# Kernel tuning notes

Measured on AMD Instinct MI355X. Metric: run time of the kernel, lower is better.

Reference implementation:

```python
import jax, jax.numpy as jnp
import numpy as np

N_STEPS = 20  # ceil((t1-t0)/dt0) with dt0=0.05 on [0,1]


def setup_inputs() -> dict:
    key = jax.random.key(0)
    ks = jax.random.split(key, 12)
    B, D, H, VF, LS, LAB = 512, 5, 128, 256, 63, 10
    Lm1 = LS - 1  # 62, effective logsig dim after dropping channel 0
    ts = jnp.linspace(0.0, 1.0, 33, dtype=jnp.float32)
    intervals = jnp.linspace(0.0, 1.0, 33, dtype=jnp.float32)
    logsig = jax.random.normal(ks[0], (32, LS), dtype=jnp.float32)
    x0 = jax.random.normal(ks[1], (B, D), dtype=jnp.float32)
    def lin(k, fan_in, shape):
        return jax.random.uniform(k, shape, jnp.float32, -1.0, 1.0) / np.sqrt(fan_in)
    return {
        "ts": ts, "logsig": logsig, "x0": x0, "intervals": intervals,
        "W_vf1": lin(ks[2], H, (VF, H)),  "b_vf1": lin(ks[3], H, (VF,)),
        "W_vf2": lin(ks[4], VF, (VF, VF)), "b_vf2": lin(ks[5], VF, (VF,)),
        "W_m": lin(ks[6], VF, (H * Lm1, VF)), "b_m": lin(ks[7], VF, (H * Lm1,)),
        "W_in": lin(ks[8], D, (H, D)),   "b_in": lin(ks[9], D, (H,)),
        "W_out": lin(ks[10], H, (LAB, H)), "b_out": lin(ks[11], H, (LAB,)),
    }


def reference(ts, logsig, x0, intervals, W_vf1, b_vf1, W_vf2, b_vf2,
              W_m, b_m, W_in, b_in, W_out, b_out):
    B = x0.shape[0]
    H = W_in.shape[0]
    L = logsig.shape[1] - 1  # channel 0 dropped

    def vector_field(t, y):
        # locate interval containing t (torch.searchsorted default = left)
        idx = jnp.clip(jnp.searchsorted(intervals[1:], t) + 1, 1, intervals.shape[0] - 1)
        seg = logsig[idx - 1, 1:]                     # (L,)
        h = jax.nn.relu(y @ W_vf1.T + b_vf1)          # (B, VF)
        h = jnp.tanh(h @ W_vf2.T + b_vf2)             # (B, VF) final_activation=tanh
        m = (h @ W_m.T + b_m).reshape(B, H, L)        # (B, H, L)
        dydt = jnp.einsum('bhl,l->bh', m, seg)
        return dydt / (intervals[idx] - intervals[idx - 1])

    y0 = x0 @ W_in.T + b_in                           # linear1
    t0, t1 = ts[0], ts[-1]
    dt = (t1 - t0) / N_STEPS

    def heun_step(y, i):
        t = t0 + i * dt
        k1 = vector_field(t, y)
        k2 = vector_field(t + dt, y + dt * k1)
        return y + 0.5 * dt * (k1 + k2), None

    yT, _ = jax.lax.scan(heun_step, y0, jnp.arange(N_STEPS, dtype=jnp.float32))
    return jax.nn.softmax(yT @ W_out.T + b_out, axis=-1)
```

## Files before the change

### kernel.cpp

```cpp
#include <hip/hip_runtime.h>

#define AW 264
#define YW 136

typedef _Float16 f16x8 __attribute__((ext_vector_type(8)));
typedef _Float16 f16x4 __attribute__((ext_vector_type(4)));
typedef __attribute__((ext_vector_type(4))) float f32x4;

__device__ __forceinline__ float fast_tanh(float x) {
    float e = __expf(2.0f * x);
    return 1.0f - 2.0f / (e + 1.0f);
}
__device__ __forceinline__ void bar_lds() {
    asm volatile("s_waitcnt lgkmcnt(0)\n\ts_barrier" ::: "memory");
}

__global__ __launch_bounds__(256) void pk_all(
    const float* __restrict__ Wvf1, const float* __restrict__ Wvf2,
    const float* __restrict__ Wm,   const float* __restrict__ bm,
    const float* __restrict__ logsig,
    _Float16* __restrict__ W1F, _Float16* __restrict__ W2F,
    _Float16* __restrict__ A3F, float* __restrict__ c_all)
{
    __shared__ float ls[32][62];
    const int b = blockIdx.x, t = threadIdx.x;
    if (b < 128) {
        int u = b * 256 + t;
        int j = u & 7, l = (u >> 3) & 63;
        int kc = (u >> 9) & 3, nt = (u >> 9) >> 2;
        int n = nt * 16 + (l & 15), k = kc * 32 + (l >> 4) * 8 + j;
        float w = Wvf1[n * 128 + k];
        _Float16 hi = (_Float16)w;
        W1F[u] = hi;
        W1F[32768 + u] = (_Float16)(w - (float)hi);
    } else if (b < 384) {
        int u = (b - 128) * 256 + t;
        int j = u & 7, l = (u >> 3) & 63;
        int kc = (u >> 9) & 7, nt = (u >> 9) >> 3;
        int n = nt * 16 + (l & 15), k = kc * 32 + (l >> 4) * 8 + j;
        float w = Wvf2[n * 256 + k];
        _Float16 hi = (_Float16)w;
        W2F[u] = hi;
        W2F[65536 + u] = (_Float16)(w - (float)hi);
    } else if (b < 896) {
        for (int e2 = t; e2 < 32 * 62; e2 += 256)
            ls[e2 / 62][e2 % 62] = logsig[(e2 / 62) * 63 + 1 + (e2 % 62)];
        __syncthreads();
        int idx = b - 384;
        int chunk = idx >> 7;
        int u = (idx & 127) * 256 + t;
        int j = u & 7, l = (u >> 3) & 63, kc = (u >> 9) & 7, nt = (u >> 12) & 7;
        int h = nt * 16 + (l & 15);
        int v = kc * 32 + (l >> 4) * 8 + j;
        int r0 = chunk * 8;
        float acc[8];
#pragma unroll
        for (int r = 0; r < 8; r++) acc[r] = 0.f;
        for (int ll = 0; ll < 62; ll++) {
            float wv2 = Wm[(h * 62 + ll) * 256 + v];
#pragma unroll
            for (int r = 0; r < 8; r++) acc[r] += wv2 * ls[r0 + r][ll];
        }
        for (int r = 0; r < 8; r++) {
            _Float16 hi = (_Float16)acc[r];
            A3F[(r0 + r) * 65536 + u] = hi;
            A3F[(r0 + r) * 65536 + 32768 + u] = (_Float16)(acc[r] - (float)hi);
        }
    } else {
        int u = (b - 896) * 256 + t;
        int r = u >> 7, h = u & 127;
        float acc = 0.f;
        for (int ll = 0; ll < 62; ll++) acc += bm[h * 62 + ll] * logsig[r * 63 + 1 + ll];
        c_all[u] = acc;
    }
}

__global__ __launch_bounds__(512, 2) void rde_main(
    const float* __restrict__ ts, const float* __restrict__ x0,
    const float* __restrict__ intervals,
    const float* __restrict__ b1g, const float* __restrict__ b2g,
    const float* __restrict__ Win, const float* __restrict__ bin,
    const float* __restrict__ Wout, const float* __restrict__ bout,
    const _Float16* __restrict__ W1F, const _Float16* __restrict__ W2F,
    const _Float16* __restrict__ A3F, const float* __restrict__ c_all,
    float* __restrict__ out)
{
    __shared__ __align__(16) _Float16 W1s[65536];
    __shared__ __align__(16) _Float16 AH[16 * AW], AL[16 * AW];
    __shared__ float Ys[16 * YW];
    __shared__ float ivl[33];
    __shared__ int   r_arr[40];
    __shared__ float s_arr[40];
    __shared__ float lg[16][12];

    const int t    = threadIdx.x;
    const int lane = t & 63;
    const int wv   = t >> 6;
    const int m16  = lane & 15;
    const int q    = lane >> 4;
    const int row0 = blockIdx.x * 16;

    if (t < 33) ivl[t] = intervals[t];
    for (int e2 = t; e2 < 8192; e2 += 512)
        ((uint4*)W1s)[e2] = ((const uint4*)W1F)[e2];
    __syncthreads();

    const float ts0 = ts[0];
    const float dt  = __fdiv_rn(ts[32] - ts0, 20.0f);

    if (t < 40) {
        int i = t >> 1;
        float tv = ts0 + (float)i * dt;
        if (t & 1) tv += dt;
        int p = 0;
        for (int j2 = 0; j2 < 32; j2++) p += (ivl[1 + j2] < tv) ? 1 : 0;
        int idx = p + 1;
        idx = idx < 1 ? 1 : idx;
        idx = idx > 32 ? 32 : idx;
        r_arr[t] = idx - 1;
        s_arr[t] = __fdiv_rn(1.0f, ivl[idx] - ivl[idx - 1]);
    }

    f32x4 b1f[2], b2f[2];
#pragma unroll
    for (int tt = 0; tt < 2; tt++) {
        b1f[tt] = *(const f32x4*)(b1g + (wv * 2 + tt) * 16 + q * 4);
        b2f[tt] = *(const f32x4*)(b2g + (wv * 2 + tt) * 16 + q * 4);
    }

    float Y[4], K1[4];
    {
        const float* xr = x0 + (row0 + m16) * 5;
        float xv[5];
#pragma unroll
        for (int d = 0; d < 5; d++) xv[d] = xr[d];
        int h0 = wv * 16 + q * 4;
        f16x4 hv, lv;
#pragma unroll
        for (int r = 0; r < 4; r++) {
            float acc = bin[h0 + r];
#pragma unroll
            for (int d = 0; d < 5; d++) acc += xv[d] * Win[(h0 + r) * 5 + d];
            Y[r] = acc;
            K1[r] = 0.f;
            _Float16 hi = (_Float16)acc;
            hv[r] = hi;
            lv[r] = (_Float16)(acc - (float)hi);
        }
        *(f16x4*)(AH + m16 * AW + h0) = hv;
        *(f16x4*)(AL + m16 * AW + h0) = lv;
    }
    __syncthreads();

#pragma unroll 1
    for (int e = 0; e < 40; e++) {
        const int half = e & 1;
        const int ri   = r_arr[e];
        const float s  = s_arr[e];
        const _Float16* ABase = A3F + ri * 65536;

        f16x8 w2a[2][4][2];
#pragma unroll
        for (int tt = 0; tt < 2; tt++)
#pragma unroll
            for (int kc = 0; kc < 4; kc++) {
                const _Float16* bp = W2F + (((wv * 2 + tt) * 8 + kc) * 64 + lane) * 8;
                w2a[tt][kc][0] = *(const f16x8*)bp;
                w2a[tt][kc][1] = *(const f16x8*)(bp + 65536);
            }
        f32x4 aA[2], aB[2], aC[2];
#pragma unroll
        for (int tt = 0; tt < 2; tt++) {
            aA[tt] = b1f[tt];
            aB[tt] = (f32x4){0.f, 0.f, 0.f, 0.f};
            aC[tt] = (f32x4){0.f, 0.f, 0.f, 0.f};
        }
#pragma unroll
        for (int kc = 0; kc < 4; kc++) {
            int ao = m16 * AW + kc * 32 + q * 8;
            f16x8 ah = *(const f16x8*)(AH + ao);
            f16x8 al = *(const f16x8*)(AL + ao);
#pragma unroll
            for (int tt = 0; tt < 2; tt++) {
                int wb = (((wv * 2 + tt) * 4 + kc) * 64 + lane) * 8;
                f16x8 bh = *(const f16x8*)(W1s + wb);
                f16x8 bl = *(const f16x8*)(W1s + 32768 + wb);
                aA[tt] = __builtin_amdgcn_mfma_f32_16x16x32_f16(bh, ah, aA[tt], 0, 0, 0);
                aB[tt] = __builtin_amdgcn_mfma_f32_16x16x32_f16(bl, ah, aB[tt], 0, 0, 0);
                aC[tt] = __builtin_amdgcn_mfma_f32_16x16x32_f16(bh, al, aC[tt], 0, 0, 0);
            }
        }
        bar_lds();
#pragma unroll
        for (int tt = 0; tt < 2; tt++) {
            int n0 = (wv * 2 + tt) * 16 + q * 4;
            f16x4 hv, lv;
#pragma unroll
            for (int r = 0; r < 4; r++) {
                float v = fmaxf(aA[tt][r] + aB[tt][r] + aC[tt][r], 0.f);
                _Float16 hi = (_Float16)v;
                hv[r] = hi;
                lv[r] = (_Float16)(v - (float)hi);
            }
            *(f16x4*)(AH + m16 * AW + n0) = hv;
            *(f16x4*)(AL + m16 * AW + n0) = lv;
        }
        bar_lds();

        f16x8 w2b[2][4][2];
#pragma unroll
        for (int tt = 0; tt < 2; tt++)
#pragma unroll
            for (int kc = 0; kc < 4; kc++) {
                const _Float16* bp = W2F + (((wv * 2 + tt) * 8 + 4 + kc) * 64 + lane) * 8;
                w2b[tt][kc][0] = *(const f16x8*)bp;
                w2b[tt][kc][1] = *(const f16x8*)(bp + 65536);
            }
#pragma unroll
        for (int tt = 0; tt < 2; tt++) {
            aA[tt] = b2f[tt];
            aB[tt] = (f32x4){0.f, 0.f, 0.f, 0.f};
            aC[tt] = (f32x4){0.f, 0.f, 0.f, 0.f};
        }
#pragma unroll
        for (int kc = 0; kc < 4; kc++) {
            int ao = m16 * AW + kc * 32 + q * 8;
            f16x8 ah = *(const f16x8*)(AH + ao);
            f16x8 al = *(const f16x8*)(AL + ao);
#pragma unroll
            for (int tt = 0; tt < 2; tt++) {
                aA[tt] = __builtin_amdgcn_mfma_f32_16x16x32_f16(w2a[tt][kc][0], ah, aA[tt], 0, 0, 0);
                aB[tt] = __builtin_amdgcn_mfma_f32_16x16x32_f16(w2a[tt][kc][1], ah, aB[tt], 0, 0, 0);
                aC[tt] = __builtin_amdgcn_mfma_f32_16x16x32_f16(w2a[tt][kc][0], al, aC[tt], 0, 0, 0);
            }
        }
        f16x8 a3a[4][2];
#pragma unroll
        for (int kc = 0; kc < 4; kc++) {
            const _Float16* bp = ABase + ((wv * 8 + kc) * 64 + lane) * 8;
            a3a[kc][0] = *(const f16x8*)bp;
            a3a[kc][1] = *(const f16x8*)(bp + 32768);
        }
        f32x4 cf = *(const f32x4*)(c_all + ri * 128 + wv * 16 + q * 4);
#pragma unroll
        for (int kc = 0; kc < 4; kc++) {
            int ao = m16 * AW + (4 + kc) * 32 + q * 8;
            f16x8 ah = *(const f16x8*)(AH + ao);
            f16x8 al = *(const f16x8*)(AL + ao);
#pragma unroll
            for (int tt = 0; tt < 2; tt++) {
                aA[tt] = __builtin_amdgcn_mfma_f32_16x16x32_f16(w2b[tt][kc][0], ah, aA[tt], 0, 0, 0);
                aB[tt] = __builtin_amdgcn_mfma_f32_16x16x32_f16(w2b[tt][kc][1], ah, aB[tt], 0, 0, 0);
                aC[tt] = __builtin_amdgcn_mfma_f32_16x16x32_f16(w2b[tt][kc][0], al, aC[tt], 0, 0, 0);
            }
        }
        f16x8 a3b[4][2];
#pragma unroll
        for (int kc = 0; kc < 4; kc++) {
            const _Float16* bp = ABase + ((wv * 8 + 4 + kc) * 64 + lane) * 8;
            a3b[kc][0] = *(const f16x8*)bp;
            a3b[kc][1] = *(const f16x8*)(bp + 32768);
        }
        bar_lds();
#pragma unroll
        for (int tt = 0; tt < 2; tt++) {
            int n0 = (wv * 2 + tt) * 16 + q * 4;
            f16x4 hv, lv;
#pragma unroll
            for (int r = 0; r < 4; r++) {
                float v = fast_tanh(aA[tt][r] + aB[tt][r] + aC[tt][r]);
                _Float16 hi = (_Float16)v;
                hv[r] = hi;
                lv[r] = (_Float16)(v - (float)hi);
            }
            *(f16x4*)(AH + m16 * AW + n0) = hv;
            *(f16x4*)(AL + m16 * AW + n0) = lv;
        }
        bar_lds();

        f32x4 kA = cf;
        f32x4 kB = (f32x4){0.f, 0.f, 0.f, 0.f};
        f32x4 kC = (f32x4){0.f, 0.f, 0.f, 0.f};
#pragma unroll
        for (int kc = 0; kc < 4; kc++) {
            int ao = m16 * AW + kc * 32 + q * 8;
            f16x8 ah = *(const f16x8*)(AH + ao);
            f16x8 al = *(const f16x8*)(AL + ao);
            kA = __builtin_amdgcn_mfma_f32_16x16x32_f16(a3a[kc][0], ah, kA, 0, 0, 0);
            kB = __builtin_amdgcn_mfma_f32_16x16x32_f16(a3a[kc][1], ah, kB, 0, 0, 0);
            kC = __builtin_amdgcn_mfma_f32_16x16x32_f16(a3a[kc][0], al, kC, 0, 0, 0);
        }
#pragma unroll
        for (int kc = 0; kc < 4; kc++) {
            int ao = m16 * AW + (4 + kc) * 32 + q * 8;
            f16x8 ah = *(const f16x8*)(AH + ao);
            f16x8 al = *(const f16x8*)(AL + ao);
            kA = __builtin_amdgcn_mfma_f32_16x16x32_f16(a3b[kc][0], ah, kA, 0, 0, 0);
            kB = __builtin_amdgcn_mfma_f32_16x16x32_f16(a3b[kc][1], ah, kB, 0, 0, 0);
            kC = __builtin_amdgcn_mfma_f32_16x16x32_f16(a3b[kc][0], al, kC, 0, 0, 0);
        }
        bar_lds();
        {
            int h0 = wv * 16 + q * 4;
            f16x4 hv, lv;
#pragma unroll
            for (int r = 0; r < 4; r++) {
                float kv = (kA[r] + kB[r] + kC[r]) * s;
                float yn;
                if (half == 0) {
                    K1[r] = kv;
                    yn = Y[r] + dt * kv;
                } else {
                    yn = Y[r] + 0.5f * dt * (K1[r] + kv);
                    Y[r] = yn;
                }
                _Float16 hi = (_Float16)yn;
                hv[r] = hi;
                lv[r] = (_Float16)(yn - (float)hi);
            }
            *(f16x4*)(AH + m16 * AW + h0) = hv;
            *(f16x4*)(AL + m16 * AW + h0) = lv;
        }
        bar_lds();
    }

#pragma unroll
    for (int r = 0; r < 4; r++)
        Ys[m16 * YW + wv * 16 + q * 4 + r] = Y[r];
    __syncthreads();
    if (t < 160) {
        int m = t / 10, c = t % 10;
        float acc = bout[c];
        for (int k = 0; k < 128; k++) acc += Ys[m * YW + k] * Wout[c * 128 + k];
        lg[m][c] = acc;
    }
    __syncthreads();
    if (t < 16) {
        float mx = -1e30f;
#pragma unroll
        for (int c = 0; c < 10; c++) mx = fmaxf(mx, lg[t][c]);
        float ex[10], sum = 0.f;
#pragma unroll
        for (int c = 0; c < 10; c++) { ex[c] = expf(lg[t][c] - mx); sum += ex[c]; }
        float inv = __fdiv_rn(1.0f, sum);
#pragma unroll
        for (int c = 0; c < 10; c++) out[(row0 + t) * 10 + c] = ex[c] * inv;
    }
}

extern "C" void kernel_launch(void* const* d_in, const int* in_sizes, int n_in,
                              void* d_out, int out_size, void* d_ws, size_t ws_size,
                              hipStream_t stream) {
    const float* ts     = (const float*)d_in[0];
    const float* logsig = (const float*)d_in[1];
    const float* x0     = (const float*)d_in[2];
    const float* ivls   = (const float*)d_in[3];
    const float* Wvf1   = (const float*)d_in[4];
    const float* bvf1   = (const float*)d_in[5];
    const float* Wvf2   = (const float*)d_in[6];
    const float* bvf2   = (const float*)d_in[7];
    const float* Wm     = (const float*)d_in[8];
    const float* bm     = (const float*)d_in[9];
    const float* Win    = (const float*)d_in[10];
    const float* bin    = (const float*)d_in[11];
    const float* Wout   = (const float*)d_in[12];
    const float* bout   = (const float*)d_in[13];

    _Float16* W1F = (_Float16*)d_ws;
    _Float16* W2F = W1F + 65536;
    _Float16* A3F = W2F + 131072;
    float* c_all = (float*)(A3F + 32 * 65536);
    float* out = (float*)d_out;

    pk_all<<<dim3(912), dim3(256), 0, stream>>>(Wvf1, Wvf2, Wm, bm, logsig,
                                                W1F, W2F, A3F, c_all);
    rde_main<<<dim3(32), dim3(512), 0, stream>>>(
        ts, x0, ivls, bvf1, bvf2, Win, bin, Wout, bout,
        W1F, W2F, A3F, c_all, out);
}
```

Baseline: 269.1 us.

## Ping-pong LDS activation buffers, keep W1 in registers, restructure A3 precompute

The main loop now alternates between two LDS activation buffer pairs, which lets it drop two of the four barriers per vector-field evaluation. The W1 split-fp16 fragments are now loaded once into registers instead of being staged in LDS, which removes the per-iteration LDS reads for the first layer. The pack kernel computes all 32 logsig rows per thread, cutting the block count and the redundant re-reads of Wm. The costs are much higher register pressure in rde_main under launch_bounds(512,2), with possible spills, and fewer parallel blocks in the precompute.

```diff
diff --git a/kernel.cpp b/kernel.cpp
--- a/kernel.cpp
+++ b/kernel.cpp
@@ -6,6 +6,7 @@
 typedef _Float16 f16x8 __attribute__((ext_vector_type(8)));
 typedef _Float16 f16x4 __attribute__((ext_vector_type(4)));
 typedef __attribute__((ext_vector_type(4))) float f32x4;
+typedef __attribute__((ext_vector_type(2))) float f32x2;
 
 __device__ __forceinline__ float fast_tanh(float x) {
     float e = __expf(2.0f * x);
@@ -42,32 +43,35 @@
         _Float16 hi = (_Float16)w;
         W2F[u] = hi;
         W2F[65536 + u] = (_Float16)(w - (float)hi);
-    } else if (b < 896) {
+    } else if (b < 512) {
         for (int e2 = t; e2 < 32 * 62; e2 += 256)
             ls[e2 / 62][e2 % 62] = logsig[(e2 / 62) * 63 + 1 + (e2 % 62)];
         __syncthreads();
-        int idx = b - 384;
-        int chunk = idx >> 7;
-        int u = (idx & 127) * 256 + t;
+        int u = (b - 384) * 256 + t;
         int j = u & 7, l = (u >> 3) & 63, kc = (u >> 9) & 7, nt = (u >> 12) & 7;
         int h = nt * 16 + (l & 15);
         int v = kc * 32 + (l >> 4) * 8 + j;
-        int r0 = chunk * 8;
-        float acc[8];
-#pragma unroll
-        for (int r = 0; r < 8; r++) acc[r] = 0.f;
-        for (int ll = 0; ll < 62; ll++) {
-            float wv2 = Wm[(h * 62 + ll) * 256 + v];
-#pragma unroll
-            for (int r = 0; r < 8; r++) acc[r] += wv2 * ls[r0 + r][ll];
-        }
-        for (int r = 0; r < 8; r++) {
+        float acc[32];
+#pragma unroll
+        for (int r = 0; r < 32; r++) acc[r] = 0.f;
+        const float* wp = Wm + (h * 62) * 256 + v;
+        for (int ll = 0; ll < 62; ll += 2) {
+            float w0 = wp[ll * 256];
+            float w1 = wp[ll * 256 + 256];
+#pragma unroll
+            for (int r = 0; r < 32; r++) {
+                f32x2 lv = *(const f32x2*)&ls[r][ll];
+                acc[r] += w0 * lv.x + w1 * lv.y;
+            }
+        }
+#pragma unroll
+        for (int r = 0; r < 32; r++) {
             _Float16 hi = (_Float16)acc[r];
-            A3F[(r0 + r) * 65536 + u] = hi;
-            A3F[(r0 + r) * 65536 + 32768 + u] = (_Float16)(acc[r] - (float)hi);
+            A3F[r * 65536 + u] = hi;
+            A3F[r * 65536 + 32768 + u] = (_Float16)(acc[r] - (float)hi);
         }
     } else {
-        int u = (b - 896) * 256 + t;
+        int u = (b - 512) * 256 + t;
         int r = u >> 7, h = u & 127;
         float acc = 0.f;
         for (int ll = 0; ll < 62; ll++) acc += bm[h * 62 + ll] * logsig[r * 63 + 1 + ll];
@@ -85,8 +89,7 @@
     const _Float16* __restrict__ A3F, const float* __restrict__ c_all,
     float* __restrict__ out)
 {
-    __shared__ __align__(16) _Float16 W1s[65536];
-    __shared__ __align__(16) _Float16 AH[16 * AW], AL[16 * AW];
+    __shared__ __align__(16) _Float16 ABUF[4][16 * AW];
     __shared__ float Ys[16 * YW];
     __shared__ float ivl[33];
     __shared__ int   r_arr[40];
@@ -100,9 +103,17 @@
     const int q    = lane >> 4;
     const int row0 = blockIdx.x * 16;
 
+    f16x8 w1h[2][4], w1l[2][4];
+#pragma unroll
+    for (int tt = 0; tt < 2; tt++)
+#pragma unroll
+        for (int kc = 0; kc < 4; kc++) {
+            const _Float16* p = W1F + (((wv * 2 + tt) * 4 + kc) * 64 + lane) * 8;
+            w1h[tt][kc] = *(const f16x8*)p;
+            w1l[tt][kc] = *(const f16x8*)(p + 32768);
+        }
+
     if (t < 33) ivl[t] = intervals[t];
-    for (int e2 = t; e2 < 8192; e2 += 512)
-        ((uint4*)W1s)[e2] = ((const uint4*)W1F)[e2];
     __syncthreads();
 
     const float ts0 = ts[0];
@@ -147,14 +158,12 @@
             hv[r] = hi;
             lv[r] = (_Float16)(acc - (float)hi);
         }
-        *(f16x4*)(AH + m16 * AW + h0) = hv;
-        *(f16x4*)(AL + m16 * AW + h0) = lv;
+        *(f16x4*)(&ABUF[0][m16 * AW + h0]) = hv;
+        *(f16x4*)(&ABUF[1][m16 * AW + h0]) = lv;
     }
     __syncthreads();
 
-#pragma unroll 1
-    for (int e = 0; e < 40; e++) {
-        const int half = e & 1;
+    auto EVAL = [&](int e, int half, int pb, int qb) {
         const int ri   = r_arr[e];
         const float s  = s_arr[e];
         const _Float16* ABase = A3F + ri * 65536;
@@ -178,19 +187,15 @@
 #pragma unroll
         for (int kc = 0; kc < 4; kc++) {
             int ao = m16 * AW + kc * 32 + q * 8;
-            f16x8 ah = *(const f16x8*)(AH + ao);
-            f16x8 al = *(const f16x8*)(AL + ao);
+            f16x8 ah = *(const f16x8*)(&ABUF[pb][ao]);
+            f16x8 al = *(const f16x8*)(&ABUF[pb + 1][ao]);
 #pragma unroll
             for (int tt = 0; tt < 2; tt++) {
-                int wb = (((wv * 2 + tt) * 4 + kc) * 64 + lane) * 8;
-                f16x8 bh = *(const f16x8*)(W1s + wb);
-                f16x8 bl = *(const f16x8*)(W1s + 32768 + wb);
-                aA[tt] = __builtin_amdgcn_mfma_f32_16x16x32_f16(bh, ah, aA[tt], 0, 0, 0);
-                aB[tt] = __builtin_amdgcn_mfma_f32_16x16x32_f16(bl, ah, aB[tt], 0, 0, 0);
-                aC[tt] = __builtin_amdgcn_mfma_f32_16x16x32_f16(bh, al, aC[tt], 0, 0, 0);
-            }
-        }
-        bar_lds();
+                aA[tt] = __builtin_amdgcn_mfma_f32_16x16x32_f16(w1h[tt][kc], ah, aA[tt], 0, 0, 0);
+                aB[tt] = __builtin_amdgcn_mfma_f32_16x16x32_f16(w1l[tt][kc], ah, aB[tt], 0, 0, 0);
+                aC[tt] = __builtin_amdgcn_mfma_f32_16x16x32_f16(w1h[tt][kc], al, aC[tt], 0, 0, 0);
+            }
+        }
 #pragma unroll
         for (int tt = 0; tt < 2; tt++) {
             int n0 = (wv * 2 + tt) * 16 + q * 4;
@@ -202,8 +207,8 @@
                 hv[r] = hi;
                 lv[r] = (_Float16)(v - (float)hi);
             }
-            *(f16x4*)(AH + m16 * AW + n0) = hv;
-            *(f16x4*)(AL + m16 * AW + n0) = lv;
+            *(f16x4*)(&ABUF[qb][m16 * AW + n0]) = hv;
+            *(f16x4*)(&ABUF[qb + 1][m16 * AW + n0]) = lv;
         }
         bar_lds();
 
@@ -225,8 +230,8 @@
 #pragma unroll
         for (int kc = 0; kc < 4; kc++) {
             int ao = m16 * AW + kc * 32 + q * 8;
-            f16x8 ah = *(const f16x8*)(AH + ao);
-            f16x8 al = *(const f16x8*)(AL + ao);
+            f16x8 ah = *(const f16x8*)(&ABUF[qb][ao]);
+            f16x8 al = *(const f16x8*)(&ABUF[qb + 1][ao]);
 #pragma unroll
             for (int tt = 0; tt < 2; tt++) {
                 aA[tt] = __builtin_amdgcn_mfma_f32_16x16x32_f16(w2a[tt][kc][0], ah, aA[tt], 0, 0, 0);
@@ -245,8 +250,8 @@
 #pragma unroll
         for (int kc = 0; kc < 4; kc++) {
             int ao = m16 * AW + (4 + kc) * 32 + q * 8;
-            f16x8 ah = *(const f16x8*)(AH + ao);
-            f16x8 al = *(const f16x8*)(AL + ao);
+            f16x8 ah = *(const f16x8*)(&ABUF[qb][ao]);
+            f16x8 al = *(const f16x8*)(&ABUF[qb + 1][ao]);
 #pragma unroll
             for (int tt = 0; tt < 2; tt++) {
                 aA[tt] = __builtin_amdgcn_mfma_f32_16x16x32_f16(w2b[tt][kc][0], ah, aA[tt], 0, 0, 0);
@@ -261,7 +266,6 @@
             a3b[kc][0] = *(const f16x8*)bp;
             a3b[kc][1] = *(const f16x8*)(bp + 32768);
         }
-        bar_lds();
 #pragma unroll
         for (int tt = 0; tt < 2; tt++) {
             int n0 = (wv * 2 + tt) * 16 + q * 4;
@@ -273,8 +277,8 @@
                 hv[r] = hi;
                 lv[r] = (_Float16)(v - (float)hi);
             }
-            *(f16x4*)(AH + m16 * AW + n0) = hv;
-            *(f16x4*)(AL + m16 * AW + n0) = lv;
+            *(f16x4*)(&ABUF[pb][m16 * AW + n0]) = hv;
+            *(f16x4*)(&ABUF[pb + 1][m16 * AW + n0]) = lv;
         }
         bar_lds();
 
@@ -284,8 +288,8 @@
 #pragma unroll
         for (int kc = 0; kc < 4; kc++) {
             int ao = m16 * AW + kc * 32 + q * 8;
-            f16x8 ah = *(const f16x8*)(AH + ao);
-            f16x8 al = *(const f16x8*)(AL + ao);
+            f16x8 ah = *(const f16x8*)(&ABUF[pb][ao]);
+            f16x8 al = *(const f16x8*)(&ABUF[pb + 1][ao]);
             kA = __builtin_amdgcn_mfma_f32_16x16x32_f16(a3a[kc][0], ah, kA, 0, 0, 0);
             kB = __builtin_amdgcn_mfma_f32_16x16x32_f16(a3a[kc][1], ah, kB, 0, 0, 0);
             kC = __builtin_amdgcn_mfma_f32_16x16x32_f16(a3a[kc][0], al, kC, 0, 0, 0);
@@ -293,13 +297,12 @@
 #pragma unroll
         for (int kc = 0; kc < 4; kc++) {
             int ao = m16 * AW + (4 + kc) * 32 + q * 8;
-            f16x8 ah = *(const f16x8*)(AH + ao);
-            f16x8 al = *(const f16x8*)(AL + ao);
+            f16x8 ah = *(const f16x8*)(&ABUF[pb][ao]);
+            f16x8 al = *(const f16x8*)(&ABUF[pb + 1][ao]);
             kA = __builtin_amdgcn_mfma_f32_16x16x32_f16(a3b[kc][0], ah, kA, 0, 0, 0);
             kB = __builtin_amdgcn_mfma_f32_16x16x32_f16(a3b[kc][1], ah, kB, 0, 0, 0);
             kC = __builtin_amdgcn_mfma_f32_16x16x32_f16(a3b[kc][0], al, kC, 0, 0, 0);
         }
-        bar_lds();
         {
             int h0 = wv * 16 + q * 4;
             f16x4 hv, lv;
@@ -318,10 +321,16 @@
                 hv[r] = hi;
                 lv[r] = (_Float16)(yn - (float)hi);
             }
-            *(f16x4*)(AH + m16 * AW + h0) = hv;
-            *(f16x4*)(AL + m16 * AW + h0) = lv;
+            *(f16x4*)(&ABUF[qb][m16 * AW + h0]) = hv;
+            *(f16x4*)(&ABUF[qb + 1][m16 * AW + h0]) = lv;
         }
         bar_lds();
+    };
+
+#pragma unroll 1
+    for (int e2 = 0; e2 < 20; e2++) {
+        EVAL(2 * e2,     0, 0, 2);
+        EVAL(2 * e2 + 1, 1, 2, 0);
     }
 
 #pragma unroll
@@ -372,7 +381,7 @@
     float* c_all = (float*)(A3F + 32 * 65536);
     float* out = (float*)d_out;
 
-    pk_all<<<dim3(912), dim3(256), 0, stream>>>(Wvf1, Wvf2, Wm, bm, logsig,
+    pk_all<<<dim3(528), dim3(256), 0, stream>>>(Wvf1, Wvf2, Wm, bm, logsig,
                                                 W1F, W2F, A3F, c_all);
     rde_main<<<dim3(32), dim3(512), 0, stream>>>(
         ts, x0, ivls, bvf1, bvf2, Win, bin, Wout, bout,
```

New measurement: 378.2 us. 40.6% more time.

## Ping-pong activation buffers with fragment layout, cut barriers, keep W1 hi in registers

Applied to the files above, without the earlier changes.

Replaces the single padded AH/AL activation tile with two ping-pong hi/lo buffer pairs stored in MFMA-fragment order, so each stage writes into the other buffer. This lets three of the five LDS barriers per evaluation be removed, because reads and writes no longer alias. The high half of W1 is held in registers and only the low half stays in LDS, which shrinks shared memory. Launch bounds drop to one block per CU, trading occupancy for more registers. The loop is unrolled by two to alternate buffers.

```diff
diff --git a/kernel.cpp b/kernel.cpp
--- a/kernel.cpp
+++ b/kernel.cpp
@@ -1,6 +1,5 @@
 #include <hip/hip_runtime.h>
 
-#define AW 264
 #define YW 136
 
 typedef _Float16 f16x8 __attribute__((ext_vector_type(8)));
@@ -13,6 +12,10 @@
 }
 __device__ __forceinline__ void bar_lds() {
     asm volatile("s_waitcnt lgkmcnt(0)\n\ts_barrier" ::: "memory");
+}
+
+__device__ __forceinline__ int fidx(int m, int c) {
+    return ((c >> 5) << 9) | (((c >> 3) & 3) << 7) | (m << 3) | (c & 7);
 }
 
 __global__ __launch_bounds__(256) void pk_all(
@@ -75,7 +78,7 @@
     }
 }
 
-__global__ __launch_bounds__(512, 2) void rde_main(
+__global__ __launch_bounds__(512, 1) void rde_main(
     const float* __restrict__ ts, const float* __restrict__ x0,
     const float* __restrict__ intervals,
     const float* __restrict__ b1g, const float* __restrict__ b2g,
@@ -85,8 +88,8 @@
     const _Float16* __restrict__ A3F, const float* __restrict__ c_all,
     float* __restrict__ out)
 {
-    __shared__ __align__(16) _Float16 W1s[65536];
-    __shared__ __align__(16) _Float16 AH[16 * AW], AL[16 * AW];
+    __shared__ __align__(16) _Float16 W1L[32768];
+    __shared__ __align__(16) _Float16 ABUF[4][4096];
     __shared__ float Ys[16 * YW];
     __shared__ float ivl[33];
     __shared__ int   r_arr[40];
@@ -100,9 +103,16 @@
     const int q    = lane >> 4;
     const int row0 = blockIdx.x * 16;
 
+    f16x8 w1h[2][4];
+#pragma unroll
+    for (int tt = 0; tt < 2; tt++)
+#pragma unroll
+        for (int kc = 0; kc < 4; kc++)
+            w1h[tt][kc] = *(const f16x8*)(W1F + ((wv * 8 + tt * 4 + kc) * 64 + lane) * 8);
+    for (int e2 = t; e2 < 4096; e2 += 512)
+        ((uint4*)W1L)[e2] = ((const uint4*)(W1F + 32768))[e2];
+
     if (t < 33) ivl[t] = intervals[t];
-    for (int e2 = t; e2 < 8192; e2 += 512)
-        ((uint4*)W1s)[e2] = ((const uint4*)W1F)[e2];
     __syncthreads();
 
     const float ts0 = ts[0];
@@ -134,37 +144,39 @@
         float xv[5];
 #pragma unroll
         for (int d = 0; d < 5; d++) xv[d] = xr[d];
-        int h0 = wv * 16 + q * 4;
+        int c0 = wv * 16 + q * 4;
         f16x4 hv, lv;
 #pragma unroll
         for (int r = 0; r < 4; r++) {
-            float acc = bin[h0 + r];
-#pragma unroll
-            for (int d = 0; d < 5; d++) acc += xv[d] * Win[(h0 + r) * 5 + d];
+            float acc = bin[c0 + r];
+#pragma unroll
+            for (int d = 0; d < 5; d++) acc += xv[d] * Win[(c0 + r) * 5 + d];
             Y[r] = acc;
             K1[r] = 0.f;
             _Float16 hi = (_Float16)acc;
             hv[r] = hi;
             lv[r] = (_Float16)(acc - (float)hi);
         }
-        *(f16x4*)(AH + m16 * AW + h0) = hv;
-        *(f16x4*)(AL + m16 * AW + h0) = lv;
+        *(f16x4*)(ABUF[0] + fidx(m16, c0)) = hv;
+        *(f16x4*)(ABUF[1] + fidx(m16, c0)) = lv;
     }
     __syncthreads();
 
-#pragma unroll 1
-    for (int e = 0; e < 40; e++) {
-        const int half = e & 1;
+    auto EVAL = [&](int e, int half, int pb, int qb) {
         const int ri   = r_arr[e];
         const float s  = s_arr[e];
         const _Float16* ABase = A3F + ri * 65536;
+        _Float16* Ph = ABUF[pb];
+        _Float16* Pl = ABUF[pb + 1];
+        _Float16* Qh = ABUF[qb];
+        _Float16* Ql = ABUF[qb + 1];
 
         f16x8 w2a[2][4][2];
 #pragma unroll
         for (int tt = 0; tt < 2; tt++)
 #pragma unroll
             for (int kc = 0; kc < 4; kc++) {
-                const _Float16* bp = W2F + (((wv * 2 + tt) * 8 + kc) * 64 + lane) * 8;
+                const _Float16* bp = W2F + ((wv * 16 + tt * 8 + kc) * 64 + lane) * 8;
                 w2a[tt][kc][0] = *(const f16x8*)bp;
                 w2a[tt][kc][1] = *(const f16x8*)(bp + 65536);
             }
@@ -177,20 +189,16 @@
         }
 #pragma unroll
         for (int kc = 0; kc < 4; kc++) {
-            int ao = m16 * AW + kc * 32 + q * 8;
-            f16x8 ah = *(const f16x8*)(AH + ao);
-            f16x8 al = *(const f16x8*)(AL + ao);
+            f16x8 ah = *(const f16x8*)(Ph + kc * 512 + lane * 8);
+            f16x8 al = *(const f16x8*)(Pl + kc * 512 + lane * 8);
 #pragma unroll
             for (int tt = 0; tt < 2; tt++) {
-                int wb = (((wv * 2 + tt) * 4 + kc) * 64 + lane) * 8;
-                f16x8 bh = *(const f16x8*)(W1s + wb);
-                f16x8 bl = *(const f16x8*)(W1s + 32768 + wb);
-                aA[tt] = __builtin_amdgcn_mfma_f32_16x16x32_f16(bh, ah, aA[tt], 0, 0, 0);
+                f16x8 bl = *(const f16x8*)(W1L + (wv * 8 + tt * 4 + kc) * 512 + lane * 8);
+                aA[tt] = __builtin_amdgcn_mfma_f32_16x16x32_f16(w1h[tt][kc], ah, aA[tt], 0, 0, 0);
                 aB[tt] = __builtin_amdgcn_mfma_f32_16x16x32_f16(bl, ah, aB[tt], 0, 0, 0);
-                aC[tt] = __builtin_amdgcn_mfma_f32_16x16x32_f16(bh, al, aC[tt], 0, 0, 0);
-            }
-        }
-        bar_lds();
+                aC[tt] = __builtin_amdgcn_mfma_f32_16x16x32_f16(w1h[tt][kc], al, aC[tt], 0, 0, 0);
+            }
+        }
 #pragma unroll
         for (int tt = 0; tt < 2; tt++) {
             int n0 = (wv * 2 + tt) * 16 + q * 4;
@@ -202,8 +210,8 @@
                 hv[r] = hi;
                 lv[r] = (_Float16)(v - (float)hi);
             }
-            *(f16x4*)(AH + m16 * AW + n0) = hv;
-            *(f16x4*)(AL + m16 * AW + n0) = lv;
+            *(f16x4*)(Qh + fidx(m16, n0)) = hv;
+            *(f16x4*)(Ql + fidx(m16, n0)) = lv;
         }
         bar_lds();
 
@@ -212,7 +220,7 @@
         for (int tt = 0; tt < 2; tt++)
 #pragma unroll
             for (int kc = 0; kc < 4; kc++) {
-                const _Float16* bp = W2F + (((wv * 2 + tt) * 8 + 4 + kc) * 64 + lane) * 8;
+                const _Float16* bp = W2F + ((wv * 16 + tt * 8 + 4 + kc) * 64 + lane) * 8;
                 w2b[tt][kc][0] = *(const f16x8*)bp;
                 w2b[tt][kc][1] = *(const f16x8*)(bp + 65536);
             }
@@ -224,9 +232,8 @@
         }
 #pragma unroll
         for (int kc = 0; kc < 4; kc++) {
-            int ao = m16 * AW + kc * 32 + q * 8;
-            f16x8 ah = *(const f16x8*)(AH + ao);
-            f16x8 al = *(const f16x8*)(AL + ao);
+            f16x8 ah = *(const f16x8*)(Qh + kc * 512 + lane * 8);
+            f16x8 al = *(const f16x8*)(Ql + kc * 512 + lane * 8);
 #pragma unroll
             for (int tt = 0; tt < 2; tt++) {
                 aA[tt] = __builtin_amdgcn_mfma_f32_16x16x32_f16(w2a[tt][kc][0], ah, aA[tt], 0, 0, 0);
@@ -244,9 +251,8 @@
         f32x4 cf = *(const f32x4*)(c_all + ri * 128 + wv * 16 + q * 4);
 #pragma unroll
         for (int kc = 0; kc < 4; kc++) {
-            int ao = m16 * AW + (4 + kc) * 32 + q * 8;
-            f16x8 ah = *(const f16x8*)(AH + ao);
-            f16x8 al = *(const f16x8*)(AL + ao);
+            f16x8 ah = *(const f16x8*)(Qh + (4 + kc) * 512 + lane * 8);
+            f16x8 al = *(const f16x8*)(Ql + (4 + kc) * 512 + lane * 8);
 #pragma unroll
             for (int tt = 0; tt < 2; tt++) {
                 aA[tt] = __builtin_amdgcn_mfma_f32_16x16x32_f16(w2b[tt][kc][0], ah, aA[tt], 0, 0, 0);
@@ -261,7 +267,6 @@
             a3b[kc][0] = *(const f16x8*)bp;
             a3b[kc][1] = *(const f16x8*)(bp + 32768);
         }
-        bar_lds();
 #pragma unroll
         for (int tt = 0; tt < 2; tt++) {
             int n0 = (wv * 2 + tt) * 16 + q * 4;
@@ -273,8 +278,8 @@
                 hv[r] = hi;
                 lv[r] = (_Float16)(v - (float)hi);
             }
-            *(f16x4*)(AH + m16 * AW + n0) = hv;
-            *(f16x4*)(AL + m16 * AW + n0) = lv;
+            *(f16x4*)(Ph + fidx(m16, n0)) = hv;
+            *(f16x4*)(Pl + fidx(m16, n0)) = lv;
         }
         bar_lds();
 
@@ -283,25 +288,22 @@
         f32x4 kC = (f32x4){0.f, 0.f, 0.f, 0.f};
 #pragma unroll
         for (int kc = 0; kc < 4; kc++) {
-            int ao = m16 * AW + kc * 32 + q * 8;
-            f16x8 ah = *(const f16x8*)(AH + ao);
-            f16x8 al = *(const f16x8*)(AL + ao);
+            f16x8 ah = *(const f16x8*)(Ph + kc * 512 + lane * 8);
+            f16x8 al = *(const f16x8*)(Pl + kc * 512 + lane * 8);
             kA = __builtin_amdgcn_mfma_f32_16x16x32_f16(a3a[kc][0], ah, kA, 0, 0, 0);
             kB = __builtin_amdgcn_mfma_f32_16x16x32_f16(a3a[kc][1], ah, kB, 0, 0, 0);
             kC = __builtin_amdgcn_mfma_f32_16x16x32_f16(a3a[kc][0], al, kC, 0, 0, 0);
         }
 #pragma unroll
         for (int kc = 0; kc < 4; kc++) {
-            int ao = m16 * AW + (4 + kc) * 32 + q * 8;
-            f16x8 ah = *(const f16x8*)(AH + ao);
-            f16x8 al = *(const f16x8*)(AL + ao);
+            f16x8 ah = *(const f16x8*)(Ph + (4 + kc) * 512 + lane * 8);
+            f16x8 al = *(const f16x8*)(Pl + (4 + kc) * 512 + lane * 8);
             kA = __builtin_amdgcn_mfma_f32_16x16x32_f16(a3b[kc][0], ah, kA, 0, 0, 0);
             kB = __builtin_amdgcn_mfma_f32_16x16x32_f16(a3b[kc][1], ah, kB, 0, 0, 0);
             kC = __builtin_amdgcn_mfma_f32_16x16x32_f16(a3b[kc][0], al, kC, 0, 0, 0);
         }
-        bar_lds();
         {
-            int h0 = wv * 16 + q * 4;
+            int c0 = wv * 16 + q * 4;
             f16x4 hv, lv;
 #pragma unroll
             for (int r = 0; r < 4; r++) {
@@ -318,10 +320,16 @@
                 hv[r] = hi;
                 lv[r] = (_Float16)(yn - (float)hi);
             }
-            *(f16x4*)(AH + m16 * AW + h0) = hv;
-            *(f16x4*)(AL + m16 * AW + h0) = lv;
+            *(f16x4*)(Qh + fidx(m16, c0)) = hv;
+            *(f16x4*)(Ql + fidx(m16, c0)) = lv;
         }
         bar_lds();
+    };
+
+#pragma unroll 1
+    for (int e2 = 0; e2 < 20; e2++) {
+        EVAL(2 * e2,     0, 0, 2);
+        EVAL(2 * e2 + 1, 1, 2, 0);
     }
 
 #pragma unroll
```

New measurement: 316.3 us. 1.18x slower.

## Split activation LDS into separate Y and H buffers in fragment layout, drop barriers

Applied to the files above, without the earlier changes.

Replaces the padded row-major activation buffers with an MFMA-fragment-ordered layout (fidx), so each lane reads its operand with a contiguous lane*8 access. Y and hidden activations now sit in separate buffers, which removes two of the per-stage barriers that guarded write-after-read on the shared buffer. Also unrolls the precompute loops in the packing kernel. Dropping the barriers relies on the Y/H separation being enough to prevent races, and the final epilogue reuses the H buffer as scratch.

```diff
diff --git a/kernel.cpp b/kernel.cpp
--- a/kernel.cpp
+++ b/kernel.cpp
@@ -1,6 +1,5 @@
 #include <hip/hip_runtime.h>
 
-#define AW 264
 #define YW 136
 
 typedef _Float16 f16x8 __attribute__((ext_vector_type(8)));
@@ -13,6 +12,10 @@
 }
 __device__ __forceinline__ void bar_lds() {
     asm volatile("s_waitcnt lgkmcnt(0)\n\ts_barrier" ::: "memory");
+}
+
+__device__ __forceinline__ int fidx(int m, int c) {
+    return ((c >> 5) << 9) | (((c >> 3) & 3) << 7) | (m << 3) | (c & 7);
 }
 
 __global__ __launch_bounds__(256) void pk_all(
@@ -56,11 +59,13 @@
         float acc[8];
 #pragma unroll
         for (int r = 0; r < 8; r++) acc[r] = 0.f;
+#pragma unroll
         for (int ll = 0; ll < 62; ll++) {
             float wv2 = Wm[(h * 62 + ll) * 256 + v];
 #pragma unroll
             for (int r = 0; r < 8; r++) acc[r] += wv2 * ls[r0 + r][ll];
         }
+#pragma unroll
         for (int r = 0; r < 8; r++) {
             _Float16 hi = (_Float16)acc[r];
             A3F[(r0 + r) * 65536 + u] = hi;
@@ -70,6 +75,7 @@
         int u = (b - 896) * 256 + t;
         int r = u >> 7, h = u & 127;
         float acc = 0.f;
+#pragma unroll
         for (int ll = 0; ll < 62; ll++) acc += bm[h * 62 + ll] * logsig[r * 63 + 1 + ll];
         c_all[u] = acc;
     }
@@ -86,12 +92,16 @@
     float* __restrict__ out)
 {
     __shared__ __align__(16) _Float16 W1s[65536];
-    __shared__ __align__(16) _Float16 AH[16 * AW], AL[16 * AW];
-    __shared__ float Ys[16 * YW];
+    __shared__ __align__(16) _Float16 HBUF[2][4096];
+    __shared__ __align__(16) _Float16 YBUF[2][2048];
     __shared__ float ivl[33];
     __shared__ int   r_arr[40];
     __shared__ float s_arr[40];
-    __shared__ float lg[16][12];
+
+    _Float16* Hh = HBUF[0];
+    _Float16* Hl = HBUF[1];
+    _Float16* Yh = YBUF[0];
+    _Float16* Yl = YBUF[1];
 
     const int t    = threadIdx.x;
     const int lane = t & 63;
@@ -134,21 +144,21 @@
         float xv[5];
 #pragma unroll
         for (int d = 0; d < 5; d++) xv[d] = xr[d];
-        int h0 = wv * 16 + q * 4;
+        int c0 = wv * 16 + q * 4;
         f16x4 hv, lv;
 #pragma unroll
         for (int r = 0; r < 4; r++) {
-            float acc = bin[h0 + r];
-#pragma unroll
-            for (int d = 0; d < 5; d++) acc += xv[d] * Win[(h0 + r) * 5 + d];
+            float acc = bin[c0 + r];
+#pragma unroll
+            for (int d = 0; d < 5; d++) acc += xv[d] * Win[(c0 + r) * 5 + d];
             Y[r] = acc;
             K1[r] = 0.f;
             _Float16 hi = (_Float16)acc;
             hv[r] = hi;
             lv[r] = (_Float16)(acc - (float)hi);
         }
-        *(f16x4*)(AH + m16 * AW + h0) = hv;
-        *(f16x4*)(AL + m16 * AW + h0) = lv;
+        *(f16x4*)(Yh + fidx(m16, c0)) = hv;
+        *(f16x4*)(Yl + fidx(m16, c0)) = lv;
     }
     __syncthreads();
 
@@ -164,7 +174,7 @@
         for (int tt = 0; tt < 2; tt++)
 #pragma unroll
             for (int kc = 0; kc < 4; kc++) {
-                const _Float16* bp = W2F + (((wv * 2 + tt) * 8 + kc) * 64 + lane) * 8;
+                const _Float16* bp = W2F + ((wv * 16 + tt * 8 + kc) * 64 + lane) * 8;
                 w2a[tt][kc][0] = *(const f16x8*)bp;
                 w2a[tt][kc][1] = *(const f16x8*)(bp + 65536);
             }
@@ -177,12 +187,11 @@
         }
 #pragma unroll
         for (int kc = 0; kc < 4; kc++) {
-            int ao = m16 * AW + kc * 32 + q * 8;
-            f16x8 ah = *(const f16x8*)(AH + ao);
-            f16x8 al = *(const f16x8*)(AL + ao);
+            f16x8 ah = *(const f16x8*)(Yh + kc * 512 + lane * 8);
+            f16x8 al = *(const f16x8*)(Yl + kc * 512 + lane * 8);
 #pragma unroll
             for (int tt = 0; tt < 2; tt++) {
-                int wb = (((wv * 2 + tt) * 4 + kc) * 64 + lane) * 8;
+                int wb = ((wv * 8 + tt * 4 + kc) * 64 + lane) * 8;
                 f16x8 bh = *(const f16x8*)(W1s + wb);
                 f16x8 bl = *(const f16x8*)(W1s + 32768 + wb);
                 aA[tt] = __builtin_amdgcn_mfma_f32_16x16x32_f16(bh, ah, aA[tt], 0, 0, 0);
@@ -190,7 +199,6 @@
                 aC[tt] = __builtin_amdgcn_mfma_f32_16x16x32_f16(bh, al, aC[tt], 0, 0, 0);
             }
         }
-        bar_lds();
 #pragma unroll
         for (int tt = 0; tt < 2; tt++) {
             int n0 = (wv * 2 + tt) * 16 + q * 4;
@@ -202,8 +210,8 @@
                 hv[r] = hi;
                 lv[r] = (_Float16)(v - (float)hi);
             }
-            *(f16x4*)(AH + m16 * AW + n0) = hv;
-            *(f16x4*)(AL + m16 * AW + n0) = lv;
+            *(f16x4*)(Hh + fidx(m16, n0)) = hv;
+            *(f16x4*)(Hl + fidx(m16, n0)) = lv;
         }
         bar_lds();
 
@@ -212,7 +220,7 @@
         for (int tt = 0; tt < 2; tt++)
 #pragma unroll
             for (int kc = 0; kc < 4; kc++) {
-                const _Float16* bp = W2F + (((wv * 2 + tt) * 8 + 4 + kc) * 64 + lane) * 8;
+                const _Float16* bp = W2F + ((wv * 16 + tt * 8 + 4 + kc) * 64 + lane) * 8;
                 w2b[tt][kc][0] = *(const f16x8*)bp;
                 w2b[tt][kc][1] = *(const f16x8*)(bp + 65536);
             }
@@ -224,9 +232,8 @@
         }
 #pragma unroll
         for (int kc = 0; kc < 4; kc++) {
-            int ao = m16 * AW + kc * 32 + q * 8;
-            f16x8 ah = *(const f16x8*)(AH + ao);
-            f16x8 al = *(const f16x8*)(AL + ao);
+            f16x8 ah = *(const f16x8*)(Hh + kc * 512 + lane * 8);
+            f16x8 al = *(const f16x8*)(Hl + kc * 512 + lane * 8);
 #pragma unroll
             for (int tt = 0; tt < 2; tt++) {
                 aA[tt] = __builtin_amdgcn_mfma_f32_16x16x32_f16(w2a[tt][kc][0], ah, aA[tt], 0, 0, 0);
@@ -244,9 +251,8 @@
         f32x4 cf = *(const f32x4*)(c_all + ri * 128 + wv * 16 + q * 4);
 #pragma unroll
         for (int kc = 0; kc < 4; kc++) {
-            int ao = m16 * AW + (4 + kc) * 32 + q * 8;
-            f16x8 ah = *(const f16x8*)(AH + ao);
-            f16x8 al = *(const f16x8*)(AL + ao);
+            f16x8 ah = *(const f16x8*)(Hh + (4 + kc) * 512 + lane * 8);
+            f16x8 al = *(const f16x8*)(Hl + (4 + kc) * 512 + lane * 8);
 #pragma unroll
             for (int tt = 0; tt < 2; tt++) {
                 aA[tt] = __builtin_amdgcn_mfma_f32_16x16x32_f16(w2b[tt][kc][0], ah, aA[tt], 0, 0, 0);
@@ -273,8 +279,8 @@
                 hv[r] = hi;
                 lv[r] = (_Float16)(v - (float)hi);
             }
-            *(f16x4*)(AH + m16 * AW + n0) = hv;
-            *(f16x4*)(AL + m16 * AW + n0) = lv;
+            *(f16x4*)(Hh + fidx(m16, n0)) = hv;
+            *(f16x4*)(Hl + fidx(m16, n0)) = lv;
         }
         bar_lds();
 
@@ -283,25 +289,22 @@
         f32x4 kC = (f32x4){0.f, 0.f, 0.f, 0.f};
 #pragma unroll
         for (int kc = 0; kc < 4; kc++) {
-            int ao = m16 * AW + kc * 32 + q * 8;
-            f16x8 ah = *(const f16x8*)(AH + ao);
-            f16x8 al = *(const f16x8*)(AL + ao);
+            f16x8 ah = *(const f16x8*)(Hh + kc * 512 + lane * 8);
+            f16x8 al = *(const f16x8*)(Hl + kc * 512 + lane * 8);
             kA = __builtin_amdgcn_mfma_f32_16x16x32_f16(a3a[kc][0], ah, kA, 0, 0, 0);
             kB = __builtin_amdgcn_mfma_f32_16x16x32_f16(a3a[kc][1], ah, kB, 0, 0, 0);
             kC = __builtin_amdgcn_mfma_f32_16x16x32_f16(a3a[kc][0], al, kC, 0, 0, 0);
         }
 #pragma unroll
         for (int kc = 0; kc < 4; kc++) {
-            int ao = m16 * AW + (4 + kc) * 32 + q * 8;
-            f16x8 ah = *(const f16x8*)(AH + ao);
-            f16x8 al = *(const f16x8*)(AL + ao);
+            f16x8 ah = *(const f16x8*)(Hh + (4 + kc) * 512 + lane * 8);
+            f16x8 al = *(const f16x8*)(Hl + (4 + kc) * 512 + lane * 8);
             kA = __builtin_amdgcn_mfma_f32_16x16x32_f16(a3b[kc][0], ah, kA, 0, 0, 0);
             kB = __builtin_amdgcn_mfma_f32_16x16x32_f16(a3b[kc][1], ah, kB, 0, 0, 0);
             kC = __builtin_amdgcn_mfma_f32_16x16x32_f16(a3b[kc][0], al, kC, 0, 0, 0);
         }
-        bar_lds();
         {
-            int h0 = wv * 16 + q * 4;
+            int c0 = wv * 16 + q * 4;
             f16x4 hv, lv;
 #pragma unroll
             for (int r = 0; r < 4; r++) {
@@ -318,12 +321,14 @@
                 hv[r] = hi;
                 lv[r] = (_Float16)(yn - (float)hi);
             }
-            *(f16x4*)(AH + m16 * AW + h0) = hv;
-            *(f16x4*)(AL + m16 * AW + h0) = lv;
+            *(f16x4*)(Yh + fidx(m16, c0)) = hv;
+            *(f16x4*)(Yl + fidx(m16, c0)) = lv;
         }
         bar_lds();
     }
 
+    float* Ys  = (float*)&HBUF[0][0];
+    float* lgp = (float*)&HBUF[0][0] + 16 * YW;
 #pragma unroll
     for (int r = 0; r < 4; r++)
         Ys[m16 * YW + wv * 16 + q * 4 + r] = Y[r];
@@ -332,16 +337,16 @@
         int m = t / 10, c = t % 10;
         float acc = bout[c];
         for (int k = 0; k < 128; k++) acc += Ys[m * YW + k] * Wout[c * 128 + k];
-        lg[m][c] = acc;
+        lgp[m * 10 + c] = acc;
     }
     __syncthreads();
     if (t < 16) {
         float mx = -1e30f;
 #pragma unroll
-        for (int c = 0; c < 10; c++) mx = fmaxf(mx, lg[t][c]);
+        for (int c = 0; c < 10; c++) mx = fmaxf(mx, lgp[t * 10 + c]);
         float ex[10], sum = 0.f;
 #pragma unroll
-        for (int c = 0; c < 10; c++) { ex[c] = expf(lg[t][c] - mx); sum += ex[c]; }
+        for (int c = 0; c < 10; c++) { ex[c] = expf(lgp[t * 10 + c] - mx); sum += ex[c]; }
         float inv = __fdiv_rn(1.0f, sum);
 #pragma unroll
         for (int c = 0; c < 10; c++) out[(row0 + t) * 10 + c] = ex[c] * inv;
```

New measurement: 254.2 us. 1.06x faster.
